# Kernel optimization log

Measured on AMD Instinct MI355X. Metric: run time of the kernel, lower is better.

## Reference

```python
import jax, jax.numpy as jnp
import numpy as np

GRIDS = ((16, 16, 16), (32, 16, 8), (8, 32, 16))  # prod == 4096 == N_p for each scale
PAIRS = ((0, 1), (0, 2), (1, 2))
KVOL = 27.0  # 3x3x3 kernel, count_include_pad=True -> always divide by 27


def _avg_pool3(x):
    # x: [B, C, d, h, w]; avg_pool3d kernel 3, stride 1, pad 1 (shape preserving)
    s = jax.lax.reduce_window(
        x, 0.0, jax.lax.add,
        window_dimensions=(1, 1, 3, 3, 3),
        window_strides=(1, 1, 1, 1, 1),
        padding=((0, 0), (0, 0), (1, 1), (1, 1), (1, 1)))
    return s / KVOL


def _window(feat, grid):
    # feat: [B, N, D] -> raw reshape into [B, D, d, h, w] (layout-mixing, faithful to torch .reshape)
    B, N, D = feat.shape
    x = feat.reshape(B, -1, *grid)
    p = _avg_pool3(x)
    return p.reshape(B, p.shape[1], -1).transpose(0, 2, 1)  # [B, N, D]


def setup_inputs() -> dict:
    key = jax.random.key(0)
    ks = jax.random.split(key, 8)
    B, N, D = 8, 4096, 512
    e0 = jax.random.normal(ks[0], (B, N, D), jnp.float32)
    e1 = jax.random.normal(ks[1], (B, N, D), jnp.float32)
    e2 = jax.random.normal(ks[2], (B, N, D), jnp.float32)
    W1 = jax.random.normal(ks[3], (3, 2 * D, D), jnp.float32) * 0.02
    b1 = jnp.zeros((3, D), jnp.float32)
    W2 = jax.random.normal(ks[4], (3, D, 1), jnp.float32) * 0.02
    b2 = jnp.zeros((3, 1), jnp.float32)
    gamma = jnp.ones((D,), jnp.float32)
    beta = jnp.zeros((D,), jnp.float32)
    Wf = jax.random.normal(ks[5], (D, D), jnp.float32) * 0.02
    bf = jnp.zeros((D,), jnp.float32)
    return dict(e0=e0, e1=e1, e2=e2, W1=W1, b1=b1, W2=W2, b2=b2,
                gamma=gamma, beta=beta, Wf=Wf, bf=bf)


def reference(e0, e1, e2, W1, b1, W2, b2, gamma, beta, Wf, bf):
    embeds = (e0, e1, e2)
    windows = [_window(embeds[s], GRIDS[s]) for s in range(3)]  # each [B, N, D]
    matched = []
    for k, (i, j) in enumerate(PAIRS):
        def mlp(c):
            h = jax.nn.relu(jnp.einsum('bne,ed->bnd', c, W1[k]) + b1[k])
            return jnp.einsum('bnd,do->bno', h, W2[k]) + b2[k]  # [B, N, 1]
        cij = jnp.concatenate([windows[i], windows[j]], axis=-1)  # [B, N, 2D]
        cji = jnp.concatenate([windows[j], windows[i]], axis=-1)
        aij = jax.nn.softmax(mlp(cij), axis=1)
        aji = jax.nn.softmax(mlp(cji), axis=1)
        matched.append(jnp.sum(aij * embeds[j], axis=1, keepdims=True))  # [B, 1, D]
        matched.append(jnp.sum(aji * embeds[i], axis=1, keepdims=True))
    fused = jnp.concatenate(list(embeds) + matched, axis=1).mean(axis=1)  # [B, D]
    mu = fused.mean(axis=-1, keepdims=True)
    var = fused.var(axis=-1, keepdims=True)
    ln = (fused - mu) / jnp.sqrt(var + 1e-5) * gamma + beta
    return ln @ Wf + bf  # [B, D]
```

## Files before the change

kernel.cpp:

```cpp
#include <hip/hip_runtime.h>
#include <hip/hip_bf16.h>

typedef unsigned short u16;
typedef __bf16 bf16x8 __attribute__((ext_vector_type(8)));
typedef float f32x4 __attribute__((ext_vector_type(4)));


static __device__ __forceinline__ u16 f2bf(float f) {
  unsigned u = __builtin_bit_cast(unsigned, f);
  unsigned r = (u + 0x7FFFu + ((u >> 16) & 1u)) >> 16;
  return (u16)r;
}

__global__ __launch_bounds__(512) void k_poolpack(const float* __restrict__ e0,
                                                  const float* __restrict__ e1,
                                                  const float* __restrict__ e2,
                                                  u16* __restrict__ packA,
                                                  int b0, int nb) {
  __shared__ __align__(16) float v[4096];
  __shared__ __align__(16) float t1[4096];
  __shared__ __align__(16) u16 outp[16384];
  int bx = blockIdx.x;
  int cg4 = bx & 127;
  int q = bx >> 7;
  int scale = q / nb;
  int lb = q - scale * nb;
  int b = b0 + lb;
  const float* eptr = scale == 0 ? e0 : (scale == 1 ? e1 : e2);
  const int LW = (scale == 0) ? 4 : (scale == 1 ? 3 : 4);
  const int LHW = (scale == 0) ? 8 : (scale == 1 ? 7 : 9);
  const int w = 1 << LW, hw = 1 << LHW;
  const int h = hw >> LW;
  const int dep = 4096 >> LHW;
  int t = threadIdx.x;
  int c0 = cg4 * 4;
  for (int ci = 0; ci < 4; ++ci) {
    const float* src = eptr + (size_t)b * 2097152 + (size_t)(c0 + ci) * 4096;
    ((float4*)v)[t] = ((const float4*)src)[t];
    ((float4*)v)[t + 512] = ((const float4*)src)[t + 512];
    __syncthreads();
    for (int j = 0; j < 8; ++j) {
      int s = t + j * 512;
      int x = s & (w - 1);
      float sum = v[s];
      if (x > 0) sum += v[s - 1];
      if (x < w - 1) sum += v[s + 1];
      t1[s] = sum;
    }
    __syncthreads();
    for (int j = 0; j < 8; ++j) {
      int s = t + j * 512;
      int y = (s >> LW) & (h - 1);
      float sum = t1[s];
      if (y > 0) sum += t1[s - w];
      if (y < h - 1) sum += t1[s + w];
      v[s] = sum;
    }
    __syncthreads();
    for (int j = 0; j < 8; ++j) {
      int s = t + j * 512;
      int z = s >> LHW;
      float sum = v[s];
      if (z > 0) sum += v[s - hw];
      if (z < dep - 1) sum += v[s + hw];
      outp[s * 4 + ci] = f2bf(sum * (1.0f / 27.0f));
    }
    __syncthreads();
  }
  int cb = c0 >> 5;
  int hi = (c0 >> 3) & 3;
  int eh = (c0 >> 2) & 1;
  size_t blk = (size_t)(lb * 3 + scale) * 2097152;
  for (int k2 = 0; k2 < 8; ++k2) {
    int s = t + k2 * 512;
    int2 val = *(const int2*)&outp[s * 4];
    size_t dst = blk + ((size_t)(s >> 4) * 16 + cb) * 512 +
                 (size_t)(hi * 16 + (s & 15)) * 8 + eh * 4;
    *(int2*)(packA + dst) = val;
  }
}

__global__ __launch_bounds__(64) void k_packW(const float* __restrict__ W1,
                                              u16* __restrict__ W1p) {
  int u = blockIdx.x;
  int kb = u & 31;
  int nb_ = (u >> 5) & 31;
  int kp = u >> 10;
  int l = threadIdx.x;
  int m = l & 15, hi = l >> 4;
  u16 tmp[8];
  for (int e = 0; e < 8; ++e) {
    int kg = kb * 32 + hi * 8 + e;
    tmp[e] = f2bf(W1[((size_t)kp * 1024 + kg) * 512 + nb_ * 16 + m]);
  }
  *(int4*)(W1p + ((size_t)u * 64 + l) * 8) = *(int4*)tmp;
}

__global__ __launch_bounds__(512) void k_gemm(const u16* __restrict__ packA,
                                              const u16* __restrict__ W1p,
                                              const float* __restrict__ b1,
                                              const float* __restrict__ W2,
                                              float* __restrict__ logits,
                                              int b0, int nb) {
  __shared__ float red[512];
  int per = gridDim.x >> 3;
  int logical = (blockIdx.x & 7) * per + (blockIdx.x >> 3);
  int dir = logical % 6;
  int group = logical / 6;
  int mt = group & 63;
  int lb = group >> 6;
  int b = b0 + lb;
  int kp = dir >> 1, sw = dir & 1;
  const int PI[3] = {0, 0, 1}, PJ[3] = {1, 2, 2};
  int pi = PI[kp], pj = PJ[kp];
  int first = sw ? pj : pi;
  int second = sw ? pi : pj;
  int t = threadIdx.x;
  int w = t >> 6;
  int l = t & 63;
  const u16* Ap1 = packA + (size_t)(lb * 3 + first) * 2097152 +
                   (size_t)mt * 32768 + (size_t)l * 8;
  const u16* Ap2 = packA + (size_t)(lb * 3 + second) * 2097152 +
                   (size_t)mt * 32768 + (size_t)l * 8;
  const u16* Bp = W1p + ((size_t)kp * 32 + w * 4) * 32 * 512 + (size_t)l * 8;
  f32x4 acc[4][4];
  for (int a = 0; a < 4; ++a)
    for (int n = 0; n < 4; ++n) acc[a][n] = (f32x4){0.f, 0.f, 0.f, 0.f};
#pragma unroll 4
  for (int ks = 0; ks < 16; ++ks) {
    bf16x8 af[4], bfr[4];
    for (int mi = 0; mi < 4; ++mi)
      af[mi] = *(const bf16x8*)(Ap1 + (size_t)(mi * 16 + ks) * 512);
    for (int ni = 0; ni < 4; ++ni)
      bfr[ni] = *(const bf16x8*)(Bp + (size_t)(ni * 32 + ks) * 512);
    for (int mi = 0; mi < 4; ++mi)
      for (int ni = 0; ni < 4; ++ni)
        acc[mi][ni] = __builtin_amdgcn_mfma_f32_16x16x32_bf16(af[mi], bfr[ni],
                                                              acc[mi][ni], 0, 0, 0);
  }
#pragma unroll 4
  for (int ks = 16; ks < 32; ++ks) {
    bf16x8 af[4], bfr[4];
    for (int mi = 0; mi < 4; ++mi)
      af[mi] = *(const bf16x8*)(Ap2 + (size_t)(mi * 16 + (ks - 16)) * 512);
    for (int ni = 0; ni < 4; ++ni)
      bfr[ni] = *(const bf16x8*)(Bp + (size_t)(ni * 32 + ks) * 512);
    for (int mi = 0; mi < 4; ++mi)
      for (int ni = 0; ni < 4; ++ni)
        acc[mi][ni] = __builtin_amdgcn_mfma_f32_16x16x32_bf16(af[mi], bfr[ni],
                                                              acc[mi][ni], 0, 0, 0);
  }
  int m = l & 15, hi = l >> 4;
  float w2v[4], b1v[4];
  for (int ni = 0; ni < 4; ++ni) {
    int n = w * 64 + ni * 16 + m;
    w2v[ni] = W2[kp * 512 + n];
    b1v[ni] = b1[kp * 512 + n];
  }
  float rs[4][4];
  for (int mi = 0; mi < 4; ++mi)
    for (int r = 0; r < 4; ++r) {
      float s = 0.f;
      for (int ni = 0; ni < 4; ++ni) {
        float h = acc[mi][ni][r] + b1v[ni];
        s += fmaxf(h, 0.f) * w2v[ni];
      }
      float vv = s;
      vv += __shfl_xor(vv, 1);
      vv += __shfl_xor(vv, 2);
      vv += __shfl_xor(vv, 4);
      vv += __shfl_xor(vv, 8);
      rs[mi][r] = vv;
    }
  if (m == 0) {
    for (int mi = 0; mi < 4; ++mi)
      for (int r = 0; r < 4; ++r)
        red[w * 64 + mi * 16 + hi * 4 + r] = rs[mi][r];
  }
  __syncthreads();
  if (t < 64) {
    float s = 0.f;
    for (int ww = 0; ww < 8; ++ww) s += red[ww * 64 + t];
    logits[((size_t)dir * 8 + b) * 4096 + mt * 64 + t] = s;
  }
}

__global__ __launch_bounds__(256) void k_softmax(float* __restrict__ logits) {
  __shared__ __align__(16) float buf[4096];
  __shared__ float wred[4];
  int row = blockIdx.x;
  float* p = logits + (size_t)row * 4096;
  int t = threadIdx.x;
  float lmax = -1e30f;
  for (int j = 0; j < 4; ++j) {
    float4 v = ((const float4*)p)[t + j * 256];
    v.x = fmaxf(fminf(v.x, 1e4f), -1e4f);
    v.y = fmaxf(fminf(v.y, 1e4f), -1e4f);
    v.z = fmaxf(fminf(v.z, 1e4f), -1e4f);
    v.w = fmaxf(fminf(v.w, 1e4f), -1e4f);
    ((float4*)buf)[t + j * 256] = v;
    lmax = fmaxf(lmax, fmaxf(fmaxf(v.x, v.y), fmaxf(v.z, v.w)));
  }
  for (int off = 1; off < 64; off <<= 1) lmax = fmaxf(lmax, __shfl_xor(lmax, off));
  if ((t & 63) == 0) wred[t >> 6] = lmax;
  __syncthreads();
  float gmax = fmaxf(fmaxf(wred[0], wred[1]), fmaxf(wred[2], wred[3]));
  __syncthreads();
  float lsum = 0.f;
  for (int j = 0; j < 16; ++j) {
    int s = t + j * 256;
    float ex = expf(buf[s] - gmax);
    buf[s] = ex;
    lsum += ex;
  }
  for (int off = 1; off < 64; off <<= 1) lsum += __shfl_xor(lsum, off);
  if ((t & 63) == 0) wred[t >> 6] = lsum;
  __syncthreads();
  float inv = 1.f / (wred[0] + wred[1] + wred[2] + wred[3]);
  for (int j = 0; j < 4; ++j) {
    int i4 = t + j * 256;
    float4 v = ((const float4*)buf)[i4];
    v.x *= inv; v.y *= inv; v.z *= inv; v.w *= inv;
    ((float4*)p)[i4] = v;
  }
}

__global__ void k_zero(float* __restrict__ p, int n) {
  int i = blockIdx.x * 256 + threadIdx.x;
  if (i < n) p[i] = 0.f;
}

__global__ __launch_bounds__(256) void k_matched(const float* __restrict__ e0,
                                                 const float* __restrict__ e1,
                                                 const float* __restrict__ e2,
                                                 const float* __restrict__ wts,
                                                 float* __restrict__ fused) {
  __shared__ float lw[384];
  int bx = blockIdx.x;
  int nc = bx & 63;
  int b = bx >> 6;
  int n0 = nc * 64;
  int t = threadIdx.x;
  for (int idx = t; idx < 384; idx += 256) {
    int dir = idx >> 6, nn = idx & 63;
    lw[idx] = wts[((size_t)dir * 8 + b) * 4096 + n0 + nn];
  }
  __syncthreads();
  size_t base = (size_t)b * 2097152 + (size_t)n0 * 512;
  const float2* p0 = (const float2*)(e0 + base) + t;
  const float2* p1 = (const float2*)(e1 + base) + t;
  const float2* p2 = (const float2*)(e2 + base) + t;
  float2 tot = {0.f, 0.f};
  float2 m0 = {0, 0}, m1 = {0, 0}, m2 = {0, 0}, m3 = {0, 0}, m4 = {0, 0}, m5 = {0, 0};
  for (int nn = 0; nn < 64; ++nn) {
    float2 v0 = p0[nn * 256];
    float2 v1 = p1[nn * 256];
    float2 v2 = p2[nn * 256];
    tot.x += v0.x + v1.x + v2.x;
    tot.y += v0.y + v1.y + v2.y;
    float w0 = lw[0 * 64 + nn], w1 = lw[1 * 64 + nn], w2 = lw[2 * 64 + nn];
    float w3 = lw[3 * 64 + nn], w4 = lw[4 * 64 + nn], w5 = lw[5 * 64 + nn];
    m0.x += w0 * v1.x; m0.y += w0 * v1.y;
    m1.x += w1 * v0.x; m1.y += w1 * v0.y;
    m2.x += w2 * v2.x; m2.y += w2 * v2.y;
    m3.x += w3 * v0.x; m3.y += w3 * v0.y;
    m4.x += w4 * v2.x; m4.y += w4 * v2.y;
    m5.x += w5 * v1.x; m5.y += w5 * v1.y;
  }
  float rx = tot.x + m0.x + m1.x + m2.x + m3.x + m4.x + m5.x;
  float ry = tot.y + m0.y + m1.y + m2.y + m3.y + m4.y + m5.y;
  atomicAdd(&fused[b * 512 + 2 * t], rx);
  atomicAdd(&fused[b * 512 + 2 * t + 1], ry);
}

__global__ __launch_bounds__(512) void k_final(const float* __restrict__ fused,
                                               const float* __restrict__ gamma,
                                               const float* __restrict__ beta,
                                               const float* __restrict__ Wf,
                                               const float* __restrict__ bfv,
                                               float* __restrict__ out) {
  __shared__ float lnv[512];
  __shared__ float sred[16];
  __shared__ float pred[4][128];
  int bx = blockIdx.x;
  int db = bx & 3, b = bx >> 2;
  int t = threadIdx.x;
  float f = fused[b * 512 + t] * (1.0f / 12294.0f);
  float s1 = f, s2 = f * f;
  for (int off = 1; off < 64; off <<= 1) {
    s1 += __shfl_xor(s1, off);
    s2 += __shfl_xor(s2, off);
  }
  if ((t & 63) == 0) {
    sred[(t >> 6) * 2] = s1;
    sred[(t >> 6) * 2 + 1] = s2;
  }
  __syncthreads();
  float S1 = 0.f, S2 = 0.f;
  for (int ww = 0; ww < 8; ++ww) {
    S1 += sred[ww * 2];
    S2 += sred[ww * 2 + 1];
  }
  float mu = S1 * (1.0f / 512.0f);
  float var = S2 * (1.0f / 512.0f) - mu * mu;
  float rstd = rsqrtf(var + 1e-5f);
  lnv[t] = (f - mu) * rstd * gamma[t] + beta[t];
  __syncthreads();
  int dt = t & 127, eq = t >> 7;
  int d = db * 128 + dt;
  float acc = 0.f;
  for (int e = eq * 128; e < eq * 128 + 128; ++e)
    acc += lnv[e] * Wf[(size_t)e * 512 + d];
  pred[eq][dt] = acc;
  __syncthreads();
  if (t < 128) {
    float r = pred[0][t] + pred[1][t] + pred[2][t] + pred[3][t] + bfv[db * 128 + t];
    out[b * 512 + db * 128 + t] = r;
  }
}

extern "C" void kernel_launch(void* const* d_in, const int* in_sizes, int n_in,
                              void* d_out, int out_size, void* d_ws, size_t ws_size,
                              hipStream_t stream) {
  const float* e0 = (const float*)d_in[0];
  const float* e1 = (const float*)d_in[1];
  const float* e2 = (const float*)d_in[2];
  const float* W1 = (const float*)d_in[3];
  const float* b1 = (const float*)d_in[4];
  const float* W2 = (const float*)d_in[5];
  const float* gamma = (const float*)d_in[7];
  const float* beta = (const float*)d_in[8];
  const float* Wf = (const float*)d_in[9];
  const float* bf = (const float*)d_in[10];

  char* ws = (char*)d_ws;
  float* fused = (float*)ws;
  float* logits = (float*)(ws + 16384);
  u16* W1p = (u16*)(ws + 802816);
  u16* packA = (u16*)(ws + 3948544);
  int nbat = 8;
  while (nbat > 1 && 3948544 + (size_t)nbat * 12582912 > ws_size) nbat >>= 1;

  hipLaunchKernelGGL(k_zero, dim3(16), dim3(256), 0, stream, fused, 4096);
  hipLaunchKernelGGL(k_packW, dim3(3072), dim3(64), 0, stream, W1, W1p);
  for (int b0 = 0; b0 < 8; b0 += nbat) {
    hipLaunchKernelGGL(k_poolpack, dim3(3 * nbat * 128), dim3(512), 0, stream,
                       e0, e1, e2, packA, b0, nbat);
    hipLaunchKernelGGL(k_gemm, dim3(6 * nbat * 64), dim3(512), 0, stream,
                       packA, W1p, b1, W2, logits, b0, nbat);
  }
  hipLaunchKernelGGL(k_softmax, dim3(48), dim3(256), 0, stream, logits);
  hipLaunchKernelGGL(k_matched, dim3(512), dim3(256), 0, stream, e0, e1, e2, logits, fused);
  hipLaunchKernelGGL(k_final, dim3(32), dim3(512), 0, stream, fused, gamma, beta, Wf, bf,
                     (float*)d_out);
}
```

Baseline: 538.1 us.

## Stage GEMM A tiles through double-buffered LDS via direct global-to-LDS loads

The GEMM previously had each of the 8 waves read the shared A tile straight from global memory. Now the block cooperatively loads A chunks into two LDS buffers with global_load_lds and overlaps each chunk's load with MFMA compute on the previous chunk, using vmcnt waits and barriers. This removes redundant global A traffic across waves and hides load latency. In exchange it adds 64KB of LDS per block, which may reduce occupancy, plus barrier overhead, and B is still read directly from global memory.

```diff
diff --git a/kernel.cpp b/kernel.cpp
--- a/kernel.cpp
+++ b/kernel.cpp
@@ -102,6 +102,7 @@
                                               const float* __restrict__ W2,
                                               float* __restrict__ logits,
                                               int b0, int nb) {
+  __shared__ __align__(16) u16 abuf[2][16384];
   __shared__ float red[512];
   int per = gridDim.x >> 3;
   int logical = (blockIdx.x & 7) * per + (blockIdx.x >> 3);
@@ -118,38 +119,72 @@
   int t = threadIdx.x;
   int w = t >> 6;
   int l = t & 63;
-  const u16* Ap1 = packA + (size_t)(lb * 3 + first) * 2097152 +
-                   (size_t)mt * 32768 + (size_t)l * 8;
-  const u16* Ap2 = packA + (size_t)(lb * 3 + second) * 2097152 +
-                   (size_t)mt * 32768 + (size_t)l * 8;
+  const u16* Abase1 = packA + (size_t)(lb * 3 + first) * 2097152 + (size_t)mt * 32768;
+  const u16* Abase2 = packA + (size_t)(lb * 3 + second) * 2097152 + (size_t)mt * 32768;
   const u16* Bp = W1p + ((size_t)kp * 32 + w * 4) * 32 * 512 + (size_t)l * 8;
+
   f32x4 acc[4][4];
   for (int a = 0; a < 4; ++a)
     for (int n = 0; n < 4; ++n) acc[a][n] = (f32x4){0.f, 0.f, 0.f, 0.f};
-#pragma unroll 4
-  for (int ks = 0; ks < 16; ++ks) {
-    bf16x8 af[4], bfr[4];
-    for (int mi = 0; mi < 4; ++mi)
-      af[mi] = *(const bf16x8*)(Ap1 + (size_t)(mi * 16 + ks) * 512);
-    for (int ni = 0; ni < 4; ++ni)
-      bfr[ni] = *(const bf16x8*)(Bp + (size_t)(ni * 32 + ks) * 512);
-    for (int mi = 0; mi < 4; ++mi)
-      for (int ni = 0; ni < 4; ++ni)
-        acc[mi][ni] = __builtin_amdgcn_mfma_f32_16x16x32_bf16(af[mi], bfr[ni],
-                                                              acc[mi][ni], 0, 0, 0);
-  }
-#pragma unroll 4
-  for (int ks = 16; ks < 32; ++ks) {
-    bf16x8 af[4], bfr[4];
-    for (int mi = 0; mi < 4; ++mi)
-      af[mi] = *(const bf16x8*)(Ap2 + (size_t)(mi * 16 + (ks - 16)) * 512);
-    for (int ni = 0; ni < 4; ++ni)
-      bfr[ni] = *(const bf16x8*)(Bp + (size_t)(ni * 32 + ks) * 512);
-    for (int mi = 0; mi < 4; ++mi)
-      for (int ni = 0; ni < 4; ++ni)
-        acc[mi][ni] = __builtin_amdgcn_mfma_f32_16x16x32_bf16(af[mi], bfr[ni],
-                                                              acc[mi][ni], 0, 0, 0);
-  }
+
+#define STAGE(BUFI, CHUNK)                                                        \
+  do {                                                                            \
+    const u16* P_ = ((CHUNK) < 2) ? Abase1 : Abase2;                              \
+    const int cc0_ = ((CHUNK) & 1) * 8;                                           \
+    for (int qi = 0; qi < 4; ++qi) {                                              \
+      int q_ = w * 4 + qi;                                                        \
+      const u16* g_ = P_ + (size_t)(q_ >> 3) * 8192 +                             \
+                      (size_t)(cc0_ + (q_ & 7)) * 512 + (size_t)l * 8;            \
+      u16* lp_ = &abuf[BUFI][q_ * 512];                                           \
+      __builtin_amdgcn_global_load_lds(                                           \
+          (const __attribute__((address_space(1))) void*)g_,                      \
+          (__attribute__((address_space(3))) void*)lp_, 16, 0, 0);                \
+    }                                                                             \
+  } while (0)
+
+#define COMPUTE(BUFI, CHUNK)                                                      \
+  do {                                                                            \
+    _Pragma("unroll")                                                             \
+    for (int kk = 0; kk < 8; ++kk) {                                              \
+      int ks_ = (CHUNK) * 8 + kk;                                                 \
+      bf16x8 af[4], bfr[4];                                                       \
+      for (int mi = 0; mi < 4; ++mi)                                              \
+        af[mi] = *(const bf16x8*)&abuf[BUFI][(mi * 8 + kk) * 512 + l * 8];        \
+      for (int ni = 0; ni < 4; ++ni)                                              \
+        bfr[ni] = *(const bf16x8*)(Bp + (size_t)(ni * 32 + ks_) * 512);           \
+      for (int mi = 0; mi < 4; ++mi)                                              \
+        for (int ni = 0; ni < 4; ++ni)                                            \
+          acc[mi][ni] = __builtin_amdgcn_mfma_f32_16x16x32_bf16(                  \
+              af[mi], bfr[ni], acc[mi][ni], 0, 0, 0);                             \
+    }                                                                             \
+  } while (0)
+
+  STAGE(0, 0);
+  STAGE(1, 1);
+  asm volatile("s_waitcnt vmcnt(4)" ::: "memory");
+  __builtin_amdgcn_sched_barrier(0);
+  __builtin_amdgcn_s_barrier();
+  COMPUTE(0, 0);
+  __builtin_amdgcn_s_barrier();
+  STAGE(0, 2);
+  asm volatile("s_waitcnt vmcnt(4)" ::: "memory");
+  __builtin_amdgcn_sched_barrier(0);
+  __builtin_amdgcn_s_barrier();
+  COMPUTE(1, 1);
+  __builtin_amdgcn_s_barrier();
+  STAGE(1, 3);
+  asm volatile("s_waitcnt vmcnt(4)" ::: "memory");
+  __builtin_amdgcn_sched_barrier(0);
+  __builtin_amdgcn_s_barrier();
+  COMPUTE(0, 2);
+  __builtin_amdgcn_s_barrier();
+  asm volatile("s_waitcnt vmcnt(0)" ::: "memory");
+  __builtin_amdgcn_sched_barrier(0);
+  __builtin_amdgcn_s_barrier();
+  COMPUTE(1, 3);
+#undef STAGE
+#undef COMPUTE
+
   int m = l & 15, hi = l >> 4;
   float w2v[4], b1v[4];
   for (int ni = 0; ni < 4; ++ni) {
```

After: 563.5 us. 4.7% more time.
